# Kernel optimization log

Measured on AMD Instinct MI355X. Metric: run time of the kernel, lower is better.

## Reference

```python
import jax, jax.numpy as jnp
import numpy as np

B, SQ, SK, H, NH = 2, 2048, 2048, 2048, 16
HD = H // NH  # 128
NEG = -1e9


def setup_inputs() -> dict:
    key = jax.random.key(0)
    ks = jax.random.split(key, 8)
    hidden_states = jax.random.normal(ks[0], (B, SQ, H), dtype=jnp.float32)
    # key already transposed/expanded for baddbmm: [B*nh, head_dim, key_len]
    k = jax.random.normal(ks[1], (B * NH, HD, SK), dtype=jnp.float32)
    v = jax.random.normal(ks[2], (B, NH, SK, HD), dtype=jnp.float32)
    # additive float causal mask [B, 1, Sq, Sk]
    causal = jnp.tril(jnp.ones((SQ, SK), dtype=bool))
    attention_mask = jnp.where(causal, 0.0, NEG).astype(jnp.float32)
    attention_mask = jnp.broadcast_to(attention_mask[None, None], (B, 1, SQ, SK))
    w_q = jax.random.normal(ks[3], (H, H), dtype=jnp.float32) * 0.02
    b_q = jnp.zeros((H,), dtype=jnp.float32)
    w_proj = jax.random.normal(ks[4], (H, H), dtype=jnp.float32) * 0.02
    b_proj = jnp.zeros((H,), dtype=jnp.float32)
    return {
        "hidden_states": hidden_states,
        "key": k,
        "value": v,
        "attention_mask": attention_mask,
        "w_q": w_q,
        "b_q": b_q,
        "w_proj": w_proj,
        "b_proj": b_proj,
    }


def reference(hidden_states, key, value, attention_mask, w_q, b_q, w_proj, b_proj):
    dtype = hidden_states.dtype
    scale = 1.0 / (HD ** 0.5)  # scale_attn_weights=True, attention_multiplier=None
    # q projection: [B, Sq, H] -> [B, nh, Sq, hd]
    q = hidden_states @ w_q.T + b_q
    q = q.reshape(B, SQ, NH, HD).transpose(0, 2, 1, 3)
    # key comes in as [B*nh, hd, Sk]
    k = key.reshape(B, NH, HD, SK)
    # scores = mask + scale * q @ k  (baddbmm with beta=1)
    scores = attention_mask + scale * jnp.einsum("bhqd,bhdk->bhqk", q, k)
    # softmax in fp32 (attention_softmax_in_fp32=True), cast back
    probs = jax.nn.softmax(scores.astype(jnp.float32), axis=-1).astype(dtype)
    # attn_pdrop=0 -> no dropout
    out = jnp.einsum("bhqk,bhkd->bhqd", probs, value)  # [B, nh, Sq, hd]
    out = out.transpose(0, 2, 1, 3).reshape(B, SQ, H)
    out = out @ w_proj.T + b_proj  # resid_pdrop=0 -> no dropout
    return out
```

## Files before the change

kernel.cpp:

```cpp
#include <hip/hip_runtime.h>
#include <hip/hip_bf16.h>

typedef __bf16 bf16;
typedef __bf16 bf16x4 __attribute__((ext_vector_type(4)));
typedef __bf16 bf16x8 __attribute__((ext_vector_type(8)));
typedef float  f32x4  __attribute__((ext_vector_type(4)));
typedef unsigned int u32;

#define B_   2
#define SQ_  2048
#define SK_  2048
#define H_   2048
#define NH_  16
#define HD_  128
#define BH_  (B_*NH_)

__device__ inline void gl_lds16(const bf16* g, bf16* l) {
  __builtin_amdgcn_global_load_lds(
      (const __attribute__((address_space(1))) u32*)(const void*)g,
      (__attribute__((address_space(3))) u32*)(void*)l,
      16, 0, 0);
}

__device__ inline float exp2_fast(float x) {
  float r; asm("v_exp_f32 %0, %1" : "=v"(r) : "v"(x)); return r;
}

__global__ __launch_bounds__(256) void cvt_f32_bf16(const float* __restrict__ in,
                                                    bf16* __restrict__ out, int n4) {
  int i = blockIdx.x * blockDim.x + threadIdx.x;
  int stride = gridDim.x * blockDim.x;
  for (; i < n4; i += stride) {
    float4 v = ((const float4*)in)[i];
    bf16x4 w; w[0] = (bf16)v.x; w[1] = (bf16)v.y; w[2] = (bf16)v.z; w[3] = (bf16)v.w;
    ((bf16x4*)out)[i] = w;
  }
}

__global__ __launch_bounds__(256) void transpose_cvt(const float* __restrict__ in,
                                                     bf16* __restrict__ out, int R, int C) {
  __shared__ float tile[64][65];
  const int bh = blockIdx.z;
  const int r0 = blockIdx.y * 64, c0 = blockIdx.x * 64;
  const float* src = in + (size_t)bh * R * C;
  bf16* dst = out + (size_t)bh * R * C;
  const int t = threadIdx.x;
  const int tx = t & 15, ty = t >> 4;
#pragma unroll
  for (int p = 0; p < 4; ++p) {
    int rr = ty + p * 16;
    float4 v = *(const float4*)&src[(size_t)(r0 + rr) * C + c0 + tx * 4];
    tile[rr][tx * 4 + 0] = v.x; tile[rr][tx * 4 + 1] = v.y;
    tile[rr][tx * 4 + 2] = v.z; tile[rr][tx * 4 + 3] = v.w;
  }
  __syncthreads();
#pragma unroll
  for (int p = 0; p < 4; ++p) {
    int cc = ty + p * 16;
    bf16x4 w;
#pragma unroll
    for (int i = 0; i < 4; ++i) w[i] = (bf16)tile[tx * 4 + i][cc];
    *(bf16x4*)&dst[(size_t)(c0 + cc) * R + r0 + tx * 4] = w;
  }
}

template <typename OutT>
__global__ __launch_bounds__(256) void gemm_bt(const bf16* __restrict__ A,
                                               const bf16* __restrict__ Bw,
                                               const float* __restrict__ bias,
                                               OutT* __restrict__ C,
                                               int M, int N, int K) {
  __shared__ bf16 Abuf[128 * 32];
  __shared__ bf16 Bbuf[128 * 32];
  const int nbn = N >> 7;
  int wg = blockIdx.x, nwg = gridDim.x;
  int swz = (nwg & 7) ? wg : ((wg & 7) * (nwg >> 3) + (wg >> 3));
  int bm = swz / nbn, bn = swz % nbn;
  const int t = threadIdx.x, lane = t & 63, wid = t >> 6;
  const int r = lane & 15, g = lane >> 4;
  const int wr = wid >> 1, wc = wid & 1;
  const size_t m0 = (size_t)bm * 128, n0 = (size_t)bn * 128;

  f32x4 acc[4][4];
#pragma unroll
  for (int m = 0; m < 4; ++m)
#pragma unroll
    for (int n = 0; n < 4; ++n) acc[m][n] = (f32x4){0.f, 0.f, 0.f, 0.f};

  for (int k0 = 0; k0 < K; k0 += 32) {
    __syncthreads();
#pragma unroll
    for (int p = 0; p < 2; ++p) {
      int c = p * 256 + t;
      int row = c >> 2, off = c & 3;
      gl_lds16(A + (m0 + row) * K + k0 + off * 8, &Abuf[(p * 256 + wid * 64) * 8]);
      gl_lds16(Bw + (n0 + row) * K + k0 + off * 8, &Bbuf[(p * 256 + wid * 64) * 8]);
    }
    __syncthreads();
    bf16x8 af[4], bfr[4];
#pragma unroll
    for (int m = 0; m < 4; ++m)
      af[m] = *(const bf16x8*)&Abuf[(wr * 64 + m * 16 + r) * 32 + g * 8];
#pragma unroll
    for (int n = 0; n < 4; ++n)
      bfr[n] = *(const bf16x8*)&Bbuf[(wc * 64 + n * 16 + r) * 32 + g * 8];
#pragma unroll
    for (int m = 0; m < 4; ++m)
#pragma unroll
      for (int n = 0; n < 4; ++n)
        acc[m][n] = __builtin_amdgcn_mfma_f32_16x16x32_bf16(af[m], bfr[n], acc[m][n], 0, 0, 0);
  }

  float bv[4];
#pragma unroll
  for (int n = 0; n < 4; ++n) bv[n] = bias[n0 + wc * 64 + n * 16 + r];
#pragma unroll
  for (int m = 0; m < 4; ++m)
#pragma unroll
    for (int n = 0; n < 4; ++n)
#pragma unroll
      for (int rr = 0; rr < 4; ++rr) {
        size_t row = m0 + wr * 64 + m * 16 + g * 4 + rr;
        size_t col = n0 + wc * 64 + n * 16 + r;
        C[row * N + col] = (OutT)(acc[m][n][rr] + bv[n]);
      }
}

__global__ __launch_bounds__(256) void flash_attn(const bf16* __restrict__ Q,
                                                  const bf16* __restrict__ Kt,
                                                  const bf16* __restrict__ Vt,
                                                  bf16* __restrict__ O) {
  __shared__ bf16 Klds[2][64 * 128];
  __shared__ bf16 Vlds[2][128 * 64];
  __shared__ bf16 Plds[4][16 * 72];

  const int id = blockIdx.x;
  const int bh = (id & 7) + 8 * ((id >> 3) >> 4);
  const int pr = (id >> 3) & 15;
  const int b = bh >> 4, h = bh & 15;
  const int t = threadIdx.x, lane = t & 63, wid = t >> 6;
  const int r = lane & 15, g = lane >> 4;

  const float SC2 = 0.08838834764831845f * 1.4426950408889634f;
  const bf16* Kbase = Kt + (size_t)bh * SK_ * HD_;
  const bf16* Vbase = Vt + (size_t)bh * HD_ * SK_;

  size_t kSrc[4], vSrc[4];
#pragma unroll
  for (int p = 0; p < 4; ++p) {
    int c = p * 256 + t;
    { int row = c >> 4, off = c & 15, src = off ^ (row & 7);
      kSrc[p] = (size_t)row * HD_ + src * 8; }
    { int row = c >> 3, off = c & 7, src = off ^ (row & 7);
      vSrc[p] = (size_t)row * SK_ + src * 8; }
  }

  int cur = 0;
#pragma unroll 1
  for (int pass = 0; pass < 2; ++pass) {
    const int qt = pass ? pr : 31 - pr;
    const int q0 = qt * 64;

    const size_t qrow = ((size_t)(b * SQ_ + q0 + wid * 16 + r)) * H_ + (size_t)h * HD_;
    bf16x8 qf[4];
#pragma unroll
    for (int kk = 0; kk < 4; ++kk) qf[kk] = *(const bf16x8*)&Q[qrow + kk * 32 + g * 8];

    f32x4 acc[8];
#pragma unroll
    for (int i = 0; i < 8; ++i) acc[i] = (f32x4){0.f, 0.f, 0.f, 0.f};
    float mrun[4], lrun[4];
#pragma unroll
    for (int i = 0; i < 4; ++i) { mrun[i] = -3.0e38f; lrun[i] = 0.f; }

#pragma unroll
    for (int p = 0; p < 4; ++p) {
      gl_lds16(Kbase + kSrc[p], &Klds[cur][(p * 256 + wid * 64) * 8]);
      gl_lds16(Vbase + vSrc[p], &Vlds[cur][(p * 256 + wid * 64) * 8]);
    }
    asm volatile("s_waitcnt vmcnt(0)" ::: "memory");
    __syncthreads();

#pragma unroll 1
    for (int st = 0; st <= qt; ++st) {
      if (st < qt) {
        const size_t ks = (size_t)(st + 1) * 64 * HD_;
        const size_t vs = (size_t)(st + 1) * 64;
#pragma unroll
        for (int p = 0; p < 4; ++p) {
          gl_lds16(Kbase + ks + kSrc[p], &Klds[cur ^ 1][(p * 256 + wid * 64) * 8]);
          gl_lds16(Vbase + vs + vSrc[p], &Vlds[cur ^ 1][(p * 256 + wid * 64) * 8]);
        }
      }

      f32x4 s[4];
#pragma unroll
      for (int sb = 0; sb < 4; ++sb) s[sb] = (f32x4){0.f, 0.f, 0.f, 0.f};
#pragma unroll
      for (int sb = 0; sb < 4; ++sb) {
        const int srow = sb * 16 + r;
#pragma unroll
        for (int kk = 0; kk < 4; ++kk) {
          bf16x8 kf = *(const bf16x8*)&Klds[cur][srow * 128 + (((kk * 4 + g) ^ (srow & 7)) * 8)];
          s[sb] = __builtin_amdgcn_mfma_f32_16x16x32_bf16(qf[kk], kf, s[sb], 0, 0, 0);
        }
      }

      float sv[4][4];
#pragma unroll
      for (int sb = 0; sb < 4; ++sb)
#pragma unroll
        for (int rr = 0; rr < 4; ++rr) {
          float x = s[sb][rr] * SC2;
          if (st == qt) {
            int s_loc = sb * 16 + r, q_loc = wid * 16 + g * 4 + rr;
            if (s_loc > q_loc) x = -3.0e38f;
          }
          sv[sb][rr] = x;
        }

      float mnew[4], corr[4];
#pragma unroll
      for (int rr = 0; rr < 4; ++rr) {
        float mx = fmaxf(fmaxf(sv[0][rr], sv[1][rr]), fmaxf(sv[2][rr], sv[3][rr]));
#pragma unroll
        for (int d = 1; d < 16; d <<= 1) mx = fmaxf(mx, __shfl_xor(mx, d));
        mnew[rr] = fmaxf(mrun[rr], mx);
        corr[rr] = exp2_fast(mrun[rr] - mnew[rr]);
        mrun[rr] = mnew[rr];
      }
      float pv[4][4];
#pragma unroll
      for (int sb = 0; sb < 4; ++sb)
#pragma unroll
        for (int rr = 0; rr < 4; ++rr) pv[sb][rr] = exp2_fast(sv[sb][rr] - mnew[rr]);
#pragma unroll
      for (int rr = 0; rr < 4; ++rr) {
        float sum = (pv[0][rr] + pv[1][rr]) + (pv[2][rr] + pv[3][rr]);
#pragma unroll
        for (int d = 1; d < 16; d <<= 1) sum += __shfl_xor(sum, d);
        lrun[rr] = lrun[rr] * corr[rr] + sum;
      }
#pragma unroll
      for (int nb = 0; nb < 8; ++nb)
#pragma unroll
        for (int rr = 0; rr < 4; ++rr) acc[nb][rr] *= corr[rr];

#pragma unroll
      for (int sb = 0; sb < 4; ++sb)
#pragma unroll
        for (int rr = 0; rr < 4; ++rr)
          Plds[wid][(g * 4 + rr) * 72 + sb * 16 + r] = (bf16)pv[sb][rr];
      bf16x8 pa[2];
#pragma unroll
      for (int k2 = 0; k2 < 2; ++k2)
        pa[k2] = *(const bf16x8*)&Plds[wid][r * 72 + k2 * 32 + g * 8];

#pragma unroll
      for (int nb = 0; nb < 8; ++nb) {
        const int drow = nb * 16 + r;
#pragma unroll
        for (int k2 = 0; k2 < 2; ++k2) {
          bf16x8 vf = *(const bf16x8*)&Vlds[cur][drow * 64 + (((k2 * 4 + g) ^ (drow & 7)) * 8)];
          acc[nb] = __builtin_amdgcn_mfma_f32_16x16x32_bf16(pa[k2], vf, acc[nb], 0, 0, 0);
        }
      }

      asm volatile("s_waitcnt vmcnt(0)" ::: "memory");
      __syncthreads();
      cur ^= 1;
    }

    float inv[4];
#pragma unroll
    for (int rr = 0; rr < 4; ++rr) inv[rr] = 1.0f / lrun[rr];
#pragma unroll
    for (int nb = 0; nb < 8; ++nb)
#pragma unroll
      for (int rr = 0; rr < 4; ++rr) {
        size_t row = (size_t)(b * SQ_ + q0 + wid * 16 + g * 4 + rr);
        O[row * H_ + (size_t)h * HD_ + nb * 16 + r] = (bf16)(acc[nb][rr] * inv[rr]);
      }
  }
}

extern "C" void kernel_launch(void* const* d_in, const int* in_sizes, int n_in,
                              void* d_out, int out_size, void* d_ws, size_t ws_size,
                              hipStream_t stream) {
  const float* hidden = (const float*)d_in[0];
  const float* key    = (const float*)d_in[1];
  const float* value  = (const float*)d_in[2];
  const float* w_q    = (const float*)d_in[4];
  const float* b_q    = (const float*)d_in[5];
  const float* w_proj = (const float*)d_in[6];
  const float* b_proj = (const float*)d_in[7];
  float* out = (float*)d_out;

  const size_t N_HID = (size_t)B_ * SQ_ * H_;
  const size_t N_W   = (size_t)H_ * H_;
  const size_t N_KV  = (size_t)BH_ * SK_ * HD_;

  bf16* hid_bf  = (bf16*)d_ws;
  bf16* wq_bf   = hid_bf + N_HID;
  bf16* wp_bf   = wq_bf + N_W;
  bf16* k_bf    = wp_bf + N_W;
  bf16* vt_bf   = k_bf + N_KV;
  bf16* q_bf    = vt_bf + N_KV;
  bf16* attn_bf = hid_bf;

  cvt_f32_bf16<<<2048, 256, 0, stream>>>(hidden, hid_bf, (int)(N_HID / 4));
  cvt_f32_bf16<<<1024, 256, 0, stream>>>(w_q, wq_bf, (int)(N_W / 4));
  cvt_f32_bf16<<<1024, 256, 0, stream>>>(w_proj, wp_bf, (int)(N_W / 4));
  transpose_cvt<<<dim3(SK_ / 64, HD_ / 64, BH_), 256, 0, stream>>>(key, k_bf, HD_, SK_);
  transpose_cvt<<<dim3(HD_ / 64, SK_ / 64, BH_), 256, 0, stream>>>(value, vt_bf, SK_, HD_);

  gemm_bt<bf16><<<(B_ * SQ_ / 128) * (H_ / 128), 256, 0, stream>>>(
      hid_bf, wq_bf, b_q, q_bf, B_ * SQ_, H_, H_);

  flash_attn<<<512, 256, 0, stream>>>(q_bf, k_bf, vt_bf, attn_bf);

  gemm_bt<float><<<(B_ * SQ_ / 128) * (H_ / 128), 256, 0, stream>>>(
      attn_bf, wp_bf, b_proj, out, B_ * SQ_, H_, H_);
}
```

Baseline: 231.3 us.

## Process both causal query tiles together sharing K/V loads, with lazy softmax rescale

The flash attention kernel now handles its two paired query tiles (31-pr and pr) in a single pass over K/V. Each K/V tile is loaded into LDS once and used by both tiles' MFMAs, instead of being reloaded in a second pass. Other changes: the softmax scale is folded into the Q projection GEMM epilogue; the running max is rescaled only when some row's max grows by more than a threshold; row sums are kept per-lane and reduced once at the end; MFMA sections get s_setprio; and launch bounds allow 2 blocks per CU. The cost is higher register pressure from two sets of accumulators. The lazy-rescale path relies on exp2 headroom for numerical safety.

```diff
diff --git a/kernel.cpp b/kernel.cpp
--- a/kernel.cpp
+++ b/kernel.cpp
@@ -69,7 +69,7 @@
                                                const bf16* __restrict__ Bw,
                                                const float* __restrict__ bias,
                                                OutT* __restrict__ C,
-                                               int M, int N, int K) {
+                                               int M, int N, int K, float osc) {
   __shared__ bf16 Abuf[128 * 32];
   __shared__ bf16 Bbuf[128 * 32];
   const int nbn = N >> 7;
@@ -122,28 +122,79 @@
       for (int rr = 0; rr < 4; ++rr) {
         size_t row = m0 + wr * 64 + m * 16 + g * 4 + rr;
         size_t col = n0 + wc * 64 + n * 16 + r;
-        C[row * N + col] = (OutT)(acc[m][n][rr] + bv[n]);
-      }
-}
-
-__global__ __launch_bounds__(256) void flash_attn(const bf16* __restrict__ Q,
-                                                  const bf16* __restrict__ Kt,
-                                                  const bf16* __restrict__ Vt,
-                                                  bf16* __restrict__ O) {
+        C[row * N + col] = (OutT)((acc[m][n][rr] + bv[n]) * osc);
+      }
+}
+
+__device__ __forceinline__ void softmax_prep(const f32x4 (&s)[4], bool diag,
+                                             int r, int g, int qbase,
+                                             float (&mrun)[4], float (&lpart)[4],
+                                             f32x4 (&acc)[8], bf16* pldsw,
+                                             bf16x8 (&pa)[2]) {
+  float sv[4][4];
+#pragma unroll
+  for (int sb = 0; sb < 4; ++sb)
+#pragma unroll
+    for (int rr = 0; rr < 4; ++rr) {
+      float x = s[sb][rr];
+      if (diag && (sb * 16 + r > qbase + g * 4 + rr)) x = -3.0e38f;
+      sv[sb][rr] = x;
+    }
+  float pm[4];
+  bool cond = true;
+#pragma unroll
+  for (int rr = 0; rr < 4; ++rr) {
+    pm[rr] = fmaxf(fmaxf(sv[0][rr], sv[1][rr]), fmaxf(sv[2][rr], sv[3][rr]));
+    cond = cond && (pm[rr] <= mrun[rr] + 10.0f);
+  }
+  if (!__all(cond ? 1 : 0)) {
+    f32x4 corrv;
+#pragma unroll
+    for (int rr = 0; rr < 4; ++rr) {
+      float mx = pm[rr];
+#pragma unroll
+      for (int d = 1; d < 16; d <<= 1) mx = fmaxf(mx, __shfl_xor(mx, d));
+      float mnew = fmaxf(mrun[rr], mx);
+      float corr = exp2_fast(mrun[rr] - mnew);
+      mrun[rr] = mnew;
+      lpart[rr] *= corr;
+      corrv[rr] = corr;
+    }
+#pragma unroll
+    for (int nb = 0; nb < 8; ++nb) acc[nb] *= corrv;
+  }
+#pragma unroll
+  for (int sb = 0; sb < 4; ++sb)
+#pragma unroll
+    for (int rr = 0; rr < 4; ++rr) {
+      float p = exp2_fast(sv[sb][rr] - mrun[rr]);
+      lpart[rr] += p;
+      pldsw[(g * 4 + rr) * 68 + sb * 16 + r] = (bf16)p;
+    }
+#pragma unroll
+  for (int k2 = 0; k2 < 2; ++k2)
+    pa[k2] = *(const bf16x8*)&pldsw[r * 68 + k2 * 32 + g * 8];
+}
+
+__global__ __launch_bounds__(256, 2) void flash_attn(const bf16* __restrict__ Q,
+                                                     const bf16* __restrict__ Kt,
+                                                     const bf16* __restrict__ Vt,
+                                                     bf16* __restrict__ O) {
   __shared__ bf16 Klds[2][64 * 128];
   __shared__ bf16 Vlds[2][128 * 64];
-  __shared__ bf16 Plds[4][16 * 72];
+  __shared__ bf16 Plds[4][16 * 68];
 
   const int id = blockIdx.x;
-  const int bh = (id & 7) + 8 * ((id >> 3) >> 4);
   const int pr = (id >> 3) & 15;
+  const int bh = (id & 7) + 8 * (id >> 7);
+  const int qtA = 31 - pr, qtB = pr;
   const int b = bh >> 4, h = bh & 15;
   const int t = threadIdx.x, lane = t & 63, wid = t >> 6;
   const int r = lane & 15, g = lane >> 4;
 
-  const float SC2 = 0.08838834764831845f * 1.4426950408889634f;
   const bf16* Kbase = Kt + (size_t)bh * SK_ * HD_;
   const bf16* Vbase = Vt + (size_t)bh * HD_ * SK_;
+  bf16* pldsw = &Plds[wid][0];
 
   size_t kSrc[4], vSrc[4];
 #pragma unroll
@@ -155,133 +206,123 @@
       vSrc[p] = (size_t)row * SK_ + src * 8; }
   }
 
+  const size_t qrowA = ((size_t)(b * SQ_ + qtA * 64 + wid * 16 + r)) * H_ + (size_t)h * HD_;
+  const size_t qrowB = ((size_t)(b * SQ_ + qtB * 64 + wid * 16 + r)) * H_ + (size_t)h * HD_;
+  bf16x8 qfA[4], qfB[4];
+#pragma unroll
+  for (int kk = 0; kk < 4; ++kk) {
+    qfA[kk] = *(const bf16x8*)&Q[qrowA + kk * 32 + g * 8];
+    qfB[kk] = *(const bf16x8*)&Q[qrowB + kk * 32 + g * 8];
+  }
+
+  f32x4 accA[8], accB[8];
+  float mrunA[4], lpartA[4], mrunB[4], lpartB[4];
+#pragma unroll
+  for (int i = 0; i < 8; ++i) { accA[i] = (f32x4){0.f,0.f,0.f,0.f}; accB[i] = (f32x4){0.f,0.f,0.f,0.f}; }
+#pragma unroll
+  for (int i = 0; i < 4; ++i) { mrunA[i] = -3.0e38f; lpartA[i] = 0.f; mrunB[i] = -3.0e38f; lpartB[i] = 0.f; }
+
   int cur = 0;
+#pragma unroll
+  for (int p = 0; p < 4; ++p) {
+    gl_lds16(Kbase + kSrc[p], &Klds[cur][(p * 256 + wid * 64) * 8]);
+    gl_lds16(Vbase + vSrc[p], &Vlds[cur][(p * 256 + wid * 64) * 8]);
+  }
+  asm volatile("s_waitcnt vmcnt(0)" ::: "memory");
+  __syncthreads();
+
 #pragma unroll 1
-  for (int pass = 0; pass < 2; ++pass) {
-    const int qt = pass ? pr : 31 - pr;
-    const int q0 = qt * 64;
-
-    const size_t qrow = ((size_t)(b * SQ_ + q0 + wid * 16 + r)) * H_ + (size_t)h * HD_;
-    bf16x8 qf[4];
-#pragma unroll
-    for (int kk = 0; kk < 4; ++kk) qf[kk] = *(const bf16x8*)&Q[qrow + kk * 32 + g * 8];
-
-    f32x4 acc[8];
-#pragma unroll
-    for (int i = 0; i < 8; ++i) acc[i] = (f32x4){0.f, 0.f, 0.f, 0.f};
-    float mrun[4], lrun[4];
-#pragma unroll
-    for (int i = 0; i < 4; ++i) { mrun[i] = -3.0e38f; lrun[i] = 0.f; }
-
-#pragma unroll
-    for (int p = 0; p < 4; ++p) {
-      gl_lds16(Kbase + kSrc[p], &Klds[cur][(p * 256 + wid * 64) * 8]);
-      gl_lds16(Vbase + vSrc[p], &Vlds[cur][(p * 256 + wid * 64) * 8]);
-    }
+  for (int st = 0; st <= qtA; ++st) {
+    if (st < qtA) {
+      const size_t ks = (size_t)(st + 1) * 64 * HD_;
+      const size_t vs = (size_t)(st + 1) * 64;
+#pragma unroll
+      for (int p = 0; p < 4; ++p) {
+        gl_lds16(Kbase + ks + kSrc[p], &Klds[cur ^ 1][(p * 256 + wid * 64) * 8]);
+        gl_lds16(Vbase + vs + vSrc[p], &Vlds[cur ^ 1][(p * 256 + wid * 64) * 8]);
+      }
+    }
+    const bool both = (st <= qtB);
+
+    f32x4 sA[4], sB[4];
+#pragma unroll
+    for (int sb = 0; sb < 4; ++sb) { sA[sb] = (f32x4){0.f,0.f,0.f,0.f}; sB[sb] = (f32x4){0.f,0.f,0.f,0.f}; }
+    __builtin_amdgcn_s_setprio(1);
+    if (both) {
+#pragma unroll
+      for (int sb = 0; sb < 4; ++sb) {
+        const int srow = sb * 16 + r;
+#pragma unroll
+        for (int kk = 0; kk < 4; ++kk) {
+          bf16x8 kf = *(const bf16x8*)&Klds[cur][srow * 128 + (((kk * 4 + g) ^ (srow & 7)) * 8)];
+          sA[sb] = __builtin_amdgcn_mfma_f32_16x16x32_bf16(qfA[kk], kf, sA[sb], 0, 0, 0);
+          sB[sb] = __builtin_amdgcn_mfma_f32_16x16x32_bf16(qfB[kk], kf, sB[sb], 0, 0, 0);
+        }
+      }
+    } else {
+#pragma unroll
+      for (int sb = 0; sb < 4; ++sb) {
+        const int srow = sb * 16 + r;
+#pragma unroll
+        for (int kk = 0; kk < 4; ++kk) {
+          bf16x8 kf = *(const bf16x8*)&Klds[cur][srow * 128 + (((kk * 4 + g) ^ (srow & 7)) * 8)];
+          sA[sb] = __builtin_amdgcn_mfma_f32_16x16x32_bf16(qfA[kk], kf, sA[sb], 0, 0, 0);
+        }
+      }
+    }
+    __builtin_amdgcn_s_setprio(0);
+
+    bf16x8 paA[2], paB[2];
+    softmax_prep(sA, st == qtA, r, g, wid * 16, mrunA, lpartA, accA, pldsw, paA);
+    if (both) softmax_prep(sB, st == qtB, r, g, wid * 16, mrunB, lpartB, accB, pldsw, paB);
+
+    __builtin_amdgcn_s_setprio(1);
+    if (both) {
+#pragma unroll
+      for (int nb = 0; nb < 8; ++nb) {
+        const int drow = nb * 16 + r;
+#pragma unroll
+        for (int k2 = 0; k2 < 2; ++k2) {
+          bf16x8 vf = *(const bf16x8*)&Vlds[cur][drow * 64 + (((k2 * 4 + g) ^ (drow & 7)) * 8)];
+          accA[nb] = __builtin_amdgcn_mfma_f32_16x16x32_bf16(paA[k2], vf, accA[nb], 0, 0, 0);
+          accB[nb] = __builtin_amdgcn_mfma_f32_16x16x32_bf16(paB[k2], vf, accB[nb], 0, 0, 0);
+        }
+      }
+    } else {
+#pragma unroll
+      for (int nb = 0; nb < 8; ++nb) {
+        const int drow = nb * 16 + r;
+#pragma unroll
+        for (int k2 = 0; k2 < 2; ++k2) {
+          bf16x8 vf = *(const bf16x8*)&Vlds[cur][drow * 64 + (((k2 * 4 + g) ^ (drow & 7)) * 8)];
+          accA[nb] = __builtin_amdgcn_mfma_f32_16x16x32_bf16(paA[k2], vf, accA[nb], 0, 0, 0);
+        }
+      }
+    }
+    __builtin_amdgcn_s_setprio(0);
+
     asm volatile("s_waitcnt vmcnt(0)" ::: "memory");
     __syncthreads();
-
-#pragma unroll 1
-    for (int st = 0; st <= qt; ++st) {
-      if (st < qt) {
-        const size_t ks = (size_t)(st + 1) * 64 * HD_;
-        const size_t vs = (size_t)(st + 1) * 64;
-#pragma unroll
-        for (int p = 0; p < 4; ++p) {
-          gl_lds16(Kbase + ks + kSrc[p], &Klds[cur ^ 1][(p * 256 + wid * 64) * 8]);
-          gl_lds16(Vbase + vs + vSrc[p], &Vlds[cur ^ 1][(p * 256 + wid * 64) * 8]);
-        }
-      }
-
-      f32x4 s[4];
-#pragma unroll
-      for (int sb = 0; sb < 4; ++sb) s[sb] = (f32x4){0.f, 0.f, 0.f, 0.f};
-#pragma unroll
-      for (int sb = 0; sb < 4; ++sb) {
-        const int srow = sb * 16 + r;
-#pragma unroll
-        for (int kk = 0; kk < 4; ++kk) {
-          bf16x8 kf = *(const bf16x8*)&Klds[cur][srow * 128 + (((kk * 4 + g) ^ (srow & 7)) * 8)];
-          s[sb] = __builtin_amdgcn_mfma_f32_16x16x32_bf16(qf[kk], kf, s[sb], 0, 0, 0);
-        }
-      }
-
-      float sv[4][4];
-#pragma unroll
-      for (int sb = 0; sb < 4; ++sb)
-#pragma unroll
-        for (int rr = 0; rr < 4; ++rr) {
-          float x = s[sb][rr] * SC2;
-          if (st == qt) {
-            int s_loc = sb * 16 + r, q_loc = wid * 16 + g * 4 + rr;
-            if (s_loc > q_loc) x = -3.0e38f;
-          }
-          sv[sb][rr] = x;
-        }
-
-      float mnew[4], corr[4];
-#pragma unroll
-      for (int rr = 0; rr < 4; ++rr) {
-        float mx = fmaxf(fmaxf(sv[0][rr], sv[1][rr]), fmaxf(sv[2][rr], sv[3][rr]));
-#pragma unroll
-        for (int d = 1; d < 16; d <<= 1) mx = fmaxf(mx, __shfl_xor(mx, d));
-        mnew[rr] = fmaxf(mrun[rr], mx);
-        corr[rr] = exp2_fast(mrun[rr] - mnew[rr]);
-        mrun[rr] = mnew[rr];
-      }
-      float pv[4][4];
-#pragma unroll
-      for (int sb = 0; sb < 4; ++sb)
-#pragma unroll
-        for (int rr = 0; rr < 4; ++rr) pv[sb][rr] = exp2_fast(sv[sb][rr] - mnew[rr]);
-#pragma unroll
-      for (int rr = 0; rr < 4; ++rr) {
-        float sum = (pv[0][rr] + pv[1][rr]) + (pv[2][rr] + pv[3][rr]);
-#pragma unroll
-        for (int d = 1; d < 16; d <<= 1) sum += __shfl_xor(sum, d);
-        lrun[rr] = lrun[rr] * corr[rr] + sum;
-      }
-#pragma unroll
-      for (int nb = 0; nb < 8; ++nb)
-#pragma unroll
-        for (int rr = 0; rr < 4; ++rr) acc[nb][rr] *= corr[rr];
-
-#pragma unroll
-      for (int sb = 0; sb < 4; ++sb)
-#pragma unroll
-        for (int rr = 0; rr < 4; ++rr)
-          Plds[wid][(g * 4 + rr) * 72 + sb * 16 + r] = (bf16)pv[sb][rr];
-      bf16x8 pa[2];
-#pragma unroll
-      for (int k2 = 0; k2 < 2; ++k2)
-        pa[k2] = *(const bf16x8*)&Plds[wid][r * 72 + k2 * 32 + g * 8];
-
-#pragma unroll
-      for (int nb = 0; nb < 8; ++nb) {
-        const int drow = nb * 16 + r;
-#pragma unroll
-        for (int k2 = 0; k2 < 2; ++k2) {
-          bf16x8 vf = *(const bf16x8*)&Vlds[cur][drow * 64 + (((k2 * 4 + g) ^ (drow & 7)) * 8)];
-          acc[nb] = __builtin_amdgcn_mfma_f32_16x16x32_bf16(pa[k2], vf, acc[nb], 0, 0, 0);
-        }
-      }
-
-      asm volatile("s_waitcnt vmcnt(0)" ::: "memory");
-      __syncthreads();
-      cur ^= 1;
-    }
-
-    float inv[4];
-#pragma unroll
-    for (int rr = 0; rr < 4; ++rr) inv[rr] = 1.0f / lrun[rr];
-#pragma unroll
-    for (int nb = 0; nb < 8; ++nb)
-#pragma unroll
-      for (int rr = 0; rr < 4; ++rr) {
-        size_t row = (size_t)(b * SQ_ + q0 + wid * 16 + g * 4 + rr);
-        O[row * H_ + (size_t)h * HD_ + nb * 16 + r] = (bf16)(acc[nb][rr] * inv[rr]);
-      }
-  }
+    cur ^= 1;
+  }
+
+  float invA[4], invB[4];
+#pragma unroll
+  for (int rr = 0; rr < 4; ++rr) {
+    float la = lpartA[rr], lb = lpartB[rr];
+#pragma unroll
+    for (int d = 1; d < 16; d <<= 1) { la += __shfl_xor(la, d); lb += __shfl_xor(lb, d); }
+    invA[rr] = 1.0f / la; invB[rr] = 1.0f / lb;
+  }
+#pragma unroll
+  for (int nb = 0; nb < 8; ++nb)
+#pragma unroll
+    for (int rr = 0; rr < 4; ++rr) {
+      size_t rowA = (size_t)(b * SQ_ + qtA * 64 + wid * 16 + g * 4 + rr);
+      size_t rowB = (size_t)(b * SQ_ + qtB * 64 + wid * 16 + g * 4 + rr);
+      O[rowA * H_ + (size_t)h * HD_ + nb * 16 + r] = (bf16)(accA[nb][rr] * invA[rr]);
+      O[rowB * H_ + (size_t)h * HD_ + nb * 16 + r] = (bf16)(accB[nb][rr] * invB[rr]);
+    }
 }
 
 extern "C" void kernel_launch(void* const* d_in, const int* in_sizes, int n_in,
@@ -299,6 +340,7 @@
   const size_t N_HID = (size_t)B_ * SQ_ * H_;
   const size_t N_W   = (size_t)H_ * H_;
   const size_t N_KV  = (size_t)BH_ * SK_ * HD_;
+  const float SC2 = 0.08838834764831845f * 1.4426950408889634f;
 
   bf16* hid_bf  = (bf16*)d_ws;
   bf16* wq_bf   = hid_bf + N_HID;
@@ -315,10 +357,10 @@
   transpose_cvt<<<dim3(HD_ / 64, SK_ / 64, BH_), 256, 0, stream>>>(value, vt_bf, SK_, HD_);
 
   gemm_bt<bf16><<<(B_ * SQ_ / 128) * (H_ / 128), 256, 0, stream>>>(
-      hid_bf, wq_bf, b_q, q_bf, B_ * SQ_, H_, H_);
+      hid_bf, wq_bf, b_q, q_bf, B_ * SQ_, H_, H_, SC2);
 
   flash_attn<<<512, 256, 0, stream>>>(q_bf, k_bf, vt_bf, attn_bf);
 
   gemm_bt<float><<<(B_ * SQ_ / 128) * (H_ / 128), 256, 0, stream>>>(
-      attn_bf, wp_bf, b_proj, out, B_ * SQ_, H_, H_);
-}
+      attn_bf, wp_bf, b_proj, out, B_ * SQ_, H_, H_, 1.0f);
+}
```

After: 235.1 us. Within noise of the previous version (+1.6%).
